# Performance work log

Measured on AMD Instinct MI355X. Metric: run time of the kernel, lower is better.

The kernel has to match this reference:

```python
import jax, jax.numpy as jnp
import numpy as np

HIDDEN = 2048
N_HEADS = 32
HEAD_DIM = HIDDEN // N_HEADS  # 64
SEQ = 2048
BATCH = 1
CHUNK = 256
TOPK = 4
THETA = 10000.0
EPS = 1e-6
NEG = jnp.float32(-1e30)


def setup_inputs() -> dict:
    key = jax.random.key(0)
    ks = jax.random.split(key, 8)
    s = 0.02
    return {
        "hidden_states": jax.random.normal(ks[0], (BATCH, SEQ, HIDDEN), jnp.float32),
        "Wq": jax.random.normal(ks[1], (HIDDEN, HIDDEN), jnp.float32) * s,
        "Wk": jax.random.normal(ks[2], (HIDDEN, HIDDEN), jnp.float32) * s,
        "Wv": jax.random.normal(ks[3], (HIDDEN, HIDDEN), jnp.float32) * s,
        "Wo": jax.random.normal(ks[4], (HIDDEN, HIDDEN), jnp.float32) * s,
        "Wg1": jax.random.normal(ks[5], (HEAD_DIM, HIDDEN), jnp.float32) * s,
        "Wg2": jax.random.normal(ks[6], (HIDDEN, HEAD_DIM), jnp.float32) * s,
        "o_norm_weight": jnp.ones((HEAD_DIM,), jnp.float32),
    }


def _rope(t):
    # t: [B, S, H, D]; non-interleaved (NeoX-style) rotary over full head dim
    D = t.shape[-1]
    pos = jnp.arange(t.shape[1], dtype=jnp.float32)
    inv_freq = 1.0 / (THETA ** (jnp.arange(0, D, 2, dtype=jnp.float32) / D))
    freqs = pos[:, None] * inv_freq[None, :]            # [S, D/2]
    cos = jnp.cos(freqs)[None, :, None, :]
    sin = jnp.sin(freqs)[None, :, None, :]
    t1, t2 = t[..., : D // 2], t[..., D // 2:]
    return jnp.concatenate([t1 * cos - t2 * sin, t1 * sin + t2 * cos], axis=-1)


def reference(hidden_states, Wq, Wk, Wv, Wo, Wg1, Wg2, o_norm_weight):
    B, S, _ = hidden_states.shape
    H, D, C = N_HEADS, HEAD_DIM, CHUNK
    NC = S // C

    q = (hidden_states @ Wq.T).reshape(B, S, H, D)
    k = (hidden_states @ Wk.T).reshape(B, S, H, D)
    v = (hidden_states @ Wv.T).reshape(B, S, H, D)
    q, k = _rope(q), _rope(k)

    # --- MoBA gating: per-chunk mean-pooled keys scored against each query ---
    kmean = k.reshape(B, NC, C, H, D).mean(axis=2)           # [B, NC, H, D]
    gate = jnp.einsum('bshd,bnhd->bhsn', q, kmean)           # [B, H, S, NC]

    pos = jnp.arange(S)
    q_chunk = pos // C                                       # [S]
    chunk_ids = jnp.arange(NC)
    future = chunk_ids[None, :] > q_chunk[:, None]           # [S, NC]
    self_blk = chunk_ids[None, :] == q_chunk[:, None]
    gate = jnp.where(future[None, None], NEG, gate)
    gate = jnp.where(self_blk[None, None], -NEG, gate)       # self block always selected

    _, topk_idx = jax.lax.top_k(gate, TOPK)                  # [B, H, S, TOPK]
    sel = jax.nn.one_hot(topk_idx, NC, dtype=jnp.bool_).any(axis=-2)  # [B, H, S, NC]

    # --- block-sparse causal attention over selected chunks ---
    allowed = jnp.take(sel, q_chunk, axis=-1)                # [B, H, S, S] key j -> chunk j//C
    causal = pos[None, :] <= pos[:, None]                    # [S, S]
    allowed = allowed & causal[None, None]

    scale = 1.0 / np.sqrt(D)
    scores = jnp.einsum('bshd,bthd->bhst', q, k) * scale
    scores = jnp.where(allowed, scores, NEG)
    p = jax.nn.softmax(scores, axis=-1)
    o = jnp.einsum('bhst,bthd->bshd', p, v)                  # [B, S, H, D]

    # --- gated RMSNorm (FusedRMSNormGated, sigmoid activation) ---
    g = ((hidden_states @ Wg1.T) @ Wg2.T).reshape(B, S, H, D)
    rms = jax.lax.rsqrt(jnp.mean(o * o, axis=-1, keepdims=True) + EPS)
    o = o * rms * o_norm_weight * jax.nn.sigmoid(g)

    return (o.reshape(B, S, H * D)) @ Wo.T
```

## Files before the change

kernel.cpp:

```cpp
#include <hip/hip_runtime.h>
#include <hip/hip_bf16.h>


typedef __attribute__((ext_vector_type(8))) short s8v;
typedef __attribute__((ext_vector_type(4))) float f4v;

#define MFMA16(A,B,C) __builtin_amdgcn_mfma_f32_16x16x32_bf16(A,B,C,0,0,0)

__device__ __forceinline__ unsigned short f2b_rne(float f){
  unsigned u = __builtin_bit_cast(unsigned, f);
  u = (u + 0x7FFFu + ((u>>16)&1u)) >> 16;
  return (unsigned short)u;
}
__device__ __forceinline__ float b2f(unsigned short h){
  unsigned u = ((unsigned)h)<<16;
  return __builtin_bit_cast(float, u);
}
__device__ __forceinline__ unsigned pack2(float a, float b){
  return (unsigned)f2b_rne(a) | ((unsigned)f2b_rne(b)<<16);
}
__device__ __forceinline__ void gld16(const void* g, void* l){
  __builtin_amdgcn_global_load_lds((const __attribute__((address_space(1))) void*)g,
                                   (__attribute__((address_space(3))) void*)l, 16, 0, 0);
}

__global__ __launch_bounds__(256) void rtab_k(double2* __restrict__ tab){
  const int i = blockIdx.x*256 + threadIdx.x;
  if (i >= 2048*32) return;
  const int d2 = i & 31, s = i >> 5;
  const double invf = 1.0 / pow(10000.0, (double)d2 / 32.0);
  const double ph = (double)s * invf;
  tab[i] = make_double2(cos(ph), sin(ph));
}

__global__ __launch_bounds__(256) void f2b4_k(const float* __restrict__ s,
                                              unsigned short* __restrict__ d, int n4){
  int i = blockIdx.x*256 + threadIdx.x;
  if (i >= n4) return;
  const float4 v = *(const float4*)(s + (size_t)i*4);
  uint2 p; p.x = pack2(v.x, v.y); p.y = pack2(v.z, v.w);
  *(uint2*)(d + (size_t)i*4) = p;
}

__global__ __launch_bounds__(256) void f2bs_k(const float* __restrict__ s,
    unsigned short* __restrict__ hi, unsigned short* __restrict__ lo, int n4){
  int i = blockIdx.x*256 + threadIdx.x;
  if (i >= n4) return;
  const float4 v = *(const float4*)(s + (size_t)i*4);
  unsigned short h0 = f2b_rne(v.x), h1 = f2b_rne(v.y), h2 = f2b_rne(v.z), h3 = f2b_rne(v.w);
  uint2 ph; ph.x = (unsigned)h0 | ((unsigned)h1<<16); ph.y = (unsigned)h2 | ((unsigned)h3<<16);
  uint2 pl; pl.x = pack2(v.x - b2f(h0), v.y - b2f(h1));
  pl.y = pack2(v.z - b2f(h2), v.w - b2f(h3));
  *(uint2*)(hi + (size_t)i*4) = ph;
  *(uint2*)(lo + (size_t)i*4) = pl;
}

__global__ __launch_bounds__(128) void wsum_k(const float* __restrict__ hs,
    const double2* __restrict__ tab, double* __restrict__ AcT, double* __restrict__ AsT){
  const int n = blockIdx.x, cq = blockIdx.y;
  const int c = cq*128 + threadIdx.x;
  double ac[32] = {}, as_[32] = {};
  for (int i = 0; i < 256; ++i) {
    const int s = n*256 + i;
    const double v = (double)hs[(size_t)s*2048 + c];
    #pragma unroll
    for (int d2 = 0; d2 < 32; ++d2) {
      const double2 t = tab[s*32 + d2];
      ac[d2]  += t.x*v;
      as_[d2] += t.y*v;
    }
  }
  #pragma unroll
  for (int d2 = 0; d2 < 32; ++d2) {
    AcT[(size_t)c*256 + n*32 + d2] = ac[d2]*(1.0/256.0);
    AsT[(size_t)c*256 + n*32 + d2] = as_[d2]*(1.0/256.0);
  }
}

__global__ __launch_bounds__(256) void transf_k(const float* __restrict__ in,
    float* __restrict__ out, int R, int C){
  __shared__ float t[64][65];
  const int c0 = blockIdx.x*64, r0 = blockIdx.y*64;
  const int tx = threadIdx.x & 63, ty4 = threadIdx.x >> 6;
  #pragma unroll
  for (int rr = 0; rr < 16; ++rr) {
    const int r = ty4*16 + rr;
    t[r][tx] = in[(size_t)(r0+r)*C + c0+tx];
  }
  __syncthreads();
  #pragma unroll
  for (int rr = 0; rr < 16; ++rr) {
    const int c = ty4*16 + rr;
    out[(size_t)(c0+c)*R + r0+tx] = t[tx][c];
  }
}

__global__ __launch_bounds__(1024) void kmean2_k(const double* __restrict__ AcT,
    const double* __restrict__ AsT, const float* __restrict__ WkT,
    double* __restrict__ Km){
  const int n = blockIdx.x, h = blockIdx.y;
  const int tid = threadIdx.x, d = tid & 63, p = tid >> 6;
  const int d2 = d & 31;
  const bool hiHalf = d >= 32;
  double a = 0.0, b = 0.0;
  #pragma unroll 4
  for (int c = p*128; c < p*128 + 128; ++c) {
    const double x  = AcT[(size_t)c*256 + n*32 + d2];
    const double y  = AsT[(size_t)c*256 + n*32 + d2];
    const double w1 = (double)WkT[(size_t)c*2048 + h*64 + d2];
    const double w2 = (double)WkT[(size_t)c*2048 + h*64 + d2 + 32];
    if (!hiHalf) { a += x*w1; b += y*w2; }
    else         { a += y*w1; b += x*w2; }
  }
  __shared__ double red[1024];
  red[tid] = hiHalf ? (a + b) : (a - b);
  __syncthreads();
  if (p < 8) red[tid] += red[tid + 512];
  __syncthreads();
  if (p < 4) red[tid] += red[tid + 256];
  __syncthreads();
  if (p < 2) red[tid] += red[tid + 128];
  __syncthreads();
  if (p == 0)
    Km[(size_t)(n*32 + h)*64 + d] = red[d] + red[d + 64];
}

__global__ __launch_bounds__(256) void gate_topk_k(const float* __restrict__ Qf,
    const double* __restrict__ Km, unsigned char* __restrict__ Allow,
    unsigned char* __restrict__ Flags){
  const int h = blockIdx.x, c = blockIdx.y, t = threadIdx.x;
  __shared__ double km[512];
  km[t]     = Km[((t>>6)*32 + h)*64 + (t&63)];
  km[t+256] = Km[(((t+256)>>6)*32 + h)*64 + (t&63)];
  __syncthreads();
  const int s = c*256 + t;
  const float* qp = Qf + (size_t)s*2048 + h*64;
  double g[8] = {};
  for (int d = 0; d < 64; ++d) {
    const double qv = (double)qp[d];
    #pragma unroll
    for (int n2 = 0; n2 < 8; ++n2) g[n2] += qv*km[n2*64+d];
  }
  double margin = 1e300;
  if (c >= 4) {
    unsigned pm = 0;
    double v[4];
    for (int rep = 0; rep < 4; ++rep) {
      double best = -1e308; int bi = 0;
      #pragma unroll
      for (int n2 = 0; n2 < 8; ++n2) {
        const bool take = (n2 < c) && !((pm>>n2)&1u) && (g[n2] > best);
        best = take ? g[n2] : best;
        bi   = take ? n2 : bi;
      }
      v[rep] = best; pm |= 1u<<bi;
    }
    margin = v[2] - v[3];
  }
  Flags[h*2048 + s] = (margin < 1e-3) ? 1 : 0;
  #pragma unroll
  for (int n2 = 0; n2 < 8; ++n2) if (n2 > c) g[n2] = -1e300;
  g[c] = 1e300;
  unsigned mask = 0;
  for (int rep = 0; rep < 4; ++rep) {
    double best = -1e308; int bi = 0;
    #pragma unroll
    for (int n2 = 0; n2 < 8; ++n2) {
      const bool take = !((mask>>n2)&1u) && (g[n2] > best);
      best = take ? g[n2] : best;
      bi   = take ? n2 : bi;
    }
    mask |= 1u<<bi;
  }
  Allow[h*2048 + s] = (unsigned char)mask;
}

__global__ __launch_bounds__(64) void repair_k(
    const float* __restrict__ hs, const float* __restrict__ Wq,
    const double2* __restrict__ tab, const double* __restrict__ Km,
    const unsigned char* __restrict__ Flags, unsigned char* __restrict__ Allow)
{
  const int s = blockIdx.x, d = threadIdx.x;
  __shared__ double qr[64];
  __shared__ double g8[8];
  for (int h = 0; h < 32; ++h) {
    if (!Flags[h*2048 + s]) continue;
    const float* hrow = hs + (size_t)s*2048;
    const float* wrow = Wq + (size_t)(h*64 + d)*2048;
    double a0=0,a1=0,a2=0,a3=0;
    for (int k = 0; k < 2048; k += 4) {
      a0 += (double)hrow[k]  *(double)wrow[k];
      a1 += (double)hrow[k+1]*(double)wrow[k+1];
      a2 += (double)hrow[k+2]*(double)wrow[k+2];
      a3 += (double)hrow[k+3]*(double)wrow[k+3];
    }
    qr[d] = (a0+a1)+(a2+a3);
    __syncthreads();
    const double2 t = tab[s*32 + (d&31)];
    const double rot = (d < 32) ? (qr[d]*t.x - qr[d+32]*t.y)
                                : (qr[d-32]*t.y + qr[d]*t.x);
    __syncthreads();
    qr[d] = rot;
    __syncthreads();
    if (d < 8) {
      double g = 0;
      const double* kmp = Km + (size_t)(d*32 + h)*64;
      for (int dd = 0; dd < 64; ++dd) g += qr[dd]*kmp[dd];
      g8[d] = g;
    }
    __syncthreads();
    if (d == 0) {
      const int c = s >> 8;
      double g[8];
      #pragma unroll
      for (int n2 = 0; n2 < 8; ++n2)
        g[n2] = (n2 > c) ? -1e300 : ((n2 == c) ? 1e300 : g8[n2]);
      unsigned mask = 0;
      for (int rep = 0; rep < 4; ++rep) {
        double best = -1e308; int bi = 0;
        #pragma unroll
        for (int n2 = 0; n2 < 8; ++n2) {
          const bool take = !((mask>>n2)&1u) && (g[n2] > best);
          best = take ? g[n2] : best;
          bi   = take ? n2 : bi;
        }
        mask |= 1u<<bi;
      }
      Allow[h*2048 + s] = (unsigned char)mask;
    }
    __syncthreads();
  }
}

__global__ __launch_bounds__(256) void gemm4_bt(
    const unsigned short* __restrict__ Ah, const unsigned short* __restrict__ Al,
    const unsigned short* __restrict__ Bh, const unsigned short* __restrict__ Bl,
    float* __restrict__ C, int M, int N, int K)
{
  alignas(16) __shared__ char SAh[16384];
  alignas(16) __shared__ char SAl[16384];
  alignas(16) __shared__ char SBh[16384];
  alignas(16) __shared__ char SBl[16384];
  const int t = threadIdx.x;
  const int wave = t>>6, lane = t&63, lg = lane>>4, lr = lane&15;
  const int wm = wave >> 1, wn = wave & 1;
  const int m0 = blockIdx.x*128, n0 = blockIdx.y*128;
  const unsigned short* Ahb = Ah + (size_t)m0*K;
  const unsigned short* Alb = Al + (size_t)m0*K;
  const unsigned short* Bhb = Bh + (size_t)n0*K;
  const unsigned short* Blb = Bl + (size_t)n0*K;
  f4v acc[4][4] = {};
  #pragma unroll 1
  for (int kt = 0; kt < K; kt += 64) {
    __syncthreads();
    #pragma unroll
    for (int i = 0; i < 4; ++i) {
      const size_t go = (size_t)(i*32 + (t>>3))*K + kt + (t&7)*8;
      gld16(Ahb + go, SAh + i*4096 + wave*1024);
      gld16(Alb + go, SAl + i*4096 + wave*1024);
      gld16(Bhb + go, SBh + i*4096 + wave*1024);
      gld16(Blb + go, SBl + i*4096 + wave*1024);
    }
    __syncthreads();
    #pragma unroll
    for (int kk = 0; kk < 2; ++kk) {
      s8v ah[4], al[4], bh[4], bl[4];
      #pragma unroll
      for (int i = 0; i < 4; ++i) {
        const int ro = (wm*64 + i*16 + lr)*128 + kk*64 + lg*16;
        ah[i] = *(const s8v*)&SAh[ro];
        al[i] = *(const s8v*)&SAl[ro];
      }
      #pragma unroll
      for (int j = 0; j < 4; ++j) {
        const int ro = (wn*64 + j*16 + lr)*128 + kk*64 + lg*16;
        bh[j] = *(const s8v*)&SBh[ro];
        bl[j] = *(const s8v*)&SBl[ro];
      }
      #pragma unroll
      for (int i = 0; i < 4; ++i)
        #pragma unroll
        for (int j = 0; j < 4; ++j) {
          f4v a = acc[i][j];
          a = MFMA16(ah[i], bh[j], a);
          a = MFMA16(ah[i], bl[j], a);
          a = MFMA16(al[i], bh[j], a);
          a = MFMA16(al[i], bl[j], a);
          acc[i][j] = a;
        }
    }
  }
  #pragma unroll
  for (int i = 0; i < 4; ++i)
    #pragma unroll
    for (int j = 0; j < 4; ++j) {
      const int row = m0 + wm*64 + i*16 + lg*4;
      const int col = n0 + wn*64 + j*16 + lr;
      #pragma unroll
      for (int r = 0; r < 4; ++r)
        C[(size_t)(row+r)*N + col] = acc[i][j][r];
    }
}

template<int BM, int BN, int WN, bool OUTBF>
__global__ __launch_bounds__(256) void gemm_bt(
    const unsigned short* __restrict__ A, const unsigned short* __restrict__ B,
    void* __restrict__ C, int M, int N, int K)
{
  alignas(16) __shared__ char AsB[BM*128];
  alignas(16) __shared__ char BsB[BN*128];
  const int t = threadIdx.x;
  const int wave = t>>6, lane = t&63, lg = lane>>4, lr = lane&15;
  const int wm = wave / WN, wn = wave % WN;
  const int m0 = blockIdx.x*BM, n0 = blockIdx.y*BN;
  const unsigned short* Ab = A + (size_t)m0*K;
  const unsigned short* Bb = B + (size_t)n0*K;
  f4v acc[4][4] = {};
  #pragma unroll 1
  for (int kt = 0; kt < K; kt += 64) {
    __syncthreads();
    #pragma unroll
    for (int i = 0; i < BM/32; ++i)
      gld16(Ab + (size_t)(i*32 + (t>>3))*K + kt + (t&7)*8, AsB + i*4096 + wave*1024);
    #pragma unroll
    for (int i = 0; i < BN/32; ++i)
      gld16(Bb + (size_t)(i*32 + (t>>3))*K + kt + (t&7)*8, BsB + i*4096 + wave*1024);
    __syncthreads();
    #pragma unroll
    for (int kk = 0; kk < 2; ++kk) {
      s8v af[4], bfr[4];
      #pragma unroll
      for (int i = 0; i < 4; ++i)
        af[i] = *(const s8v*)&AsB[(wm*64 + i*16 + lr)*128 + kk*64 + lg*16];
      #pragma unroll
      for (int j = 0; j < 4; ++j)
        bfr[j] = *(const s8v*)&BsB[(wn*64 + j*16 + lr)*128 + kk*64 + lg*16];
      #pragma unroll
      for (int i = 0; i < 4; ++i)
        #pragma unroll
        for (int j = 0; j < 4; ++j)
          acc[i][j] = MFMA16(af[i], bfr[j], acc[i][j]);
    }
  }
  #pragma unroll
  for (int i = 0; i < 4; ++i)
    #pragma unroll
    for (int j = 0; j < 4; ++j) {
      const int row = m0 + wm*64 + i*16 + lg*4;
      const int col = n0 + wn*64 + j*16 + lr;
      #pragma unroll
      for (int r = 0; r < 4; ++r) {
        if (OUTBF) ((unsigned short*)C)[(size_t)(row+r)*N + col] = f2b_rne(acc[i][j][r]);
        else       ((float*)C)[(size_t)(row+r)*N + col] = acc[i][j][r];
      }
    }
}

__global__ __launch_bounds__(256) void rope32q_k(float* __restrict__ Qf,
    unsigned short* __restrict__ Qb, const double2* __restrict__ tab){
  const int idx = blockIdx.x*256 + threadIdx.x;
  const int d2 = idx & 31, hh = (idx>>5)&31, s = idx>>10;
  const double2 t = tab[s*32 + d2];
  const float cs = (float)t.x, sn = (float)t.y;
  const size_t base = (size_t)s*2048 + hh*64 + d2;
  const float q1 = Qf[base], q2 = Qf[base+32];
  const float o1 = q1*cs - q2*sn, o2 = q1*sn + q2*cs;
  Qf[base] = o1; Qf[base+32] = o2;
  Qb[base] = f2b_rne(o1); Qb[base+32] = f2b_rne(o2);
}

__global__ __launch_bounds__(256) void rope32_k(const float* __restrict__ Kf,
    unsigned short* __restrict__ Kb, const double2* __restrict__ tab){
  const int idx = blockIdx.x*256 + threadIdx.x;
  const int d2 = idx & 31, hh = (idx>>5)&31, s = idx>>10;
  const double2 t = tab[s*32 + d2];
  const float cs = (float)t.x, sn = (float)t.y;
  const size_t base = (size_t)s*2048 + hh*64 + d2;
  const float k1 = Kf[base], k2 = Kf[base+32];
  Kb[base]    = f2b_rne(k1*cs - k2*sn);
  Kb[base+32] = f2b_rne(k1*sn + k2*cs);
}

__global__ __launch_bounds__(256) void vtrans_k(const float* __restrict__ V,
                                                unsigned short* __restrict__ Vt){
  __shared__ unsigned short tile[64][68];
  const int s0 = blockIdx.x*64, c0 = blockIdx.y*64;
  const int tx = threadIdx.x & 63, ty = threadIdx.x >> 6;
  #pragma unroll
  for (int rr = 0; rr < 16; ++rr) {
    const int r = ty*16 + rr;
    tile[tx][r] = f2b_rne(V[(size_t)(s0+r)*2048 + c0+tx]);
  }
  __syncthreads();
  #pragma unroll
  for (int rr = 0; rr < 16; ++rr) {
    const int cc = ty*16 + rr;
    Vt[(size_t)(c0+cc)*2048 + s0+tx] = tile[cc][tx];
  }
}

__global__ __launch_bounds__(256) void attn_k(
    const unsigned short* __restrict__ Qb, const unsigned short* __restrict__ Kb,
    const unsigned short* __restrict__ Vt, const float* __restrict__ Gf,
    const unsigned char* __restrict__ Allow, const float* __restrict__ Wn,
    unsigned short* __restrict__ Ob)
{
  const int h = blockIdx.x, c = blockIdx.y;
  const int t = threadIdx.x, wave = t>>6, lane = t&63, lg = lane>>4, lr = lane&15;
  const int qbase = c*256 + (blockIdx.z*4 + wave)*16;
  const size_t qrow = (size_t)(qbase + lr);
  const s8v qf0 = *(const s8v*)&Qb[qrow*2048 + h*64 + lg*8];
  const s8v qf1 = *(const s8v*)&Qb[qrow*2048 + h*64 + 32 + lg*8];
  const unsigned am = Allow[h*2048 + qrow];
  const int q = qbase + lr;
  const int laneA = ((lg&1)<<5) + lr;
  const bool hiSel = lg >= 2;

  float mx = -1e30f, ls = 0.f;
  f4v ot[4] = {};

  for (int n = 0; n <= c; ++n) {
    if (!__ballot((am>>n)&1u)) continue;
    const int okc = (am>>n)&1;
    #pragma unroll 1
    for (int t4 = 0; t4 < 4; ++t4) {
      const int kb0 = n*256 + t4*64;
      s8v kf[4][2];
      #pragma unroll
      for (int i = 0; i < 4; ++i) {
        const size_t krow = (size_t)(kb0 + i*16 + lr);
        kf[i][0] = *(const s8v*)&Kb[krow*2048 + h*64 + lg*8];
        kf[i][1] = *(const s8v*)&Kb[krow*2048 + h*64 + 32 + lg*8];
      }
      f4v st[4];
      #pragma unroll
      for (int i = 0; i < 4; ++i) {
        f4v zz = {};
        zz = MFMA16(kf[i][0], qf0, zz);
        st[i] = MFMA16(kf[i][1], qf1, zz);
      }
      float cm = -__builtin_inff();
      #pragma unroll
      for (int i = 0; i < 4; ++i)
        #pragma unroll
        for (int r = 0; r < 4; ++r) {
          float v = st[i][r]*0.125f;
          const int key = kb0 + i*16 + lg*4 + r;
          const bool ok = okc && (n != c || key <= q);
          v = ok ? v : -__builtin_inff();
          st[i][r] = v;
          cm = fmaxf(cm, v);
        }
      cm = fmaxf(cm, __shfl_xor(cm, 16));
      cm = fmaxf(cm, __shfl_xor(cm, 32));
      const float nm = fmaxf(mx, cm);
      const float al = __expf(mx - nm);
      mx = nm;
      uint2 w[4];
      float ps = 0.f;
      #pragma unroll
      for (int i = 0; i < 4; ++i) {
        const float p0 = __expf(st[i][0]-mx);
        const float p1 = __expf(st[i][1]-mx);
        const float p2 = __expf(st[i][2]-mx);
        const float p3 = __expf(st[i][3]-mx);
        ps += (p0+p1)+(p2+p3);
        w[i].x = pack2(p0,p1);
        w[i].y = pack2(p2,p3);
      }
      ps += __shfl_xor(ps, 16);
      ps += __shfl_xor(ps, 32);
      ls = ls*al + ps;
      #pragma unroll
      for (int jd = 0; jd < 4; ++jd) ot[jd] *= al;
      #pragma unroll
      for (int kk = 0; kk < 2; ++kk) {
        const unsigned a0x = __shfl(w[2*kk].x,   laneA);
        const unsigned a0y = __shfl(w[2*kk].y,   laneA);
        const unsigned b0x = __shfl(w[2*kk].x,   laneA+16);
        const unsigned b0y = __shfl(w[2*kk].y,   laneA+16);
        const unsigned a1x = __shfl(w[2*kk+1].x, laneA);
        const unsigned a1y = __shfl(w[2*kk+1].y, laneA);
        const unsigned b1x = __shfl(w[2*kk+1].x, laneA+16);
        const unsigned b1y = __shfl(w[2*kk+1].y, laneA+16);
        uint4 uu;
        uu.x = hiSel ? a1x : a0x;
        uu.y = hiSel ? a1y : a0y;
        uu.z = hiSel ? b1x : b0x;
        uu.w = hiSel ? b1y : b0y;
        const s8v pfr = __builtin_bit_cast(s8v, uu);
        s8v vfr[4];
        #pragma unroll
        for (int jd = 0; jd < 4; ++jd)
          vfr[jd] = *(const s8v*)&Vt[(size_t)(h*64 + jd*16 + lr)*2048 + kb0 + kk*32 + lg*8];
        #pragma unroll
        for (int jd = 0; jd < 4; ++jd)
          ot[jd] = MFMA16(vfr[jd], pfr, ot[jd]);
      }
    }
  }
  const float inv_ = 1.0f/ls;
  float ssum = 0.f;
  #pragma unroll
  for (int jd = 0; jd < 4; ++jd)
    #pragma unroll
    for (int r = 0; r < 4; ++r) {
      const float o = ot[jd][r]*inv_;
      ot[jd][r] = o;
      ssum += o*o;
    }
  ssum += __shfl_xor(ssum, 16);
  ssum += __shfl_xor(ssum, 32);
  const float rmsv = rsqrtf(ssum*(1.0f/64.0f) + 1e-6f);
  #pragma unroll
  for (int jd = 0; jd < 4; ++jd) {
    const float4 w4 = *(const float4*)&Wn[jd*16 + lg*4];
    const float4 g4 = *(const float4*)&Gf[qrow*2048 + h*64 + jd*16 + lg*4];
    const float o0 = ot[jd][0]*rmsv*w4.x*(1.0f/(1.0f+__expf(-g4.x)));
    const float o1 = ot[jd][1]*rmsv*w4.y*(1.0f/(1.0f+__expf(-g4.y)));
    const float o2 = ot[jd][2]*rmsv*w4.z*(1.0f/(1.0f+__expf(-g4.z)));
    const float o3 = ot[jd][3]*rmsv*w4.w*(1.0f/(1.0f+__expf(-g4.w)));
    uint2 pk; pk.x = pack2(o0,o1); pk.y = pack2(o2,o3);
    *(uint2*)&Ob[qrow*2048 + h*64 + jd*16 + lg*4] = pk;
  }
}

extern "C" void kernel_launch(void* const* d_in, const int* in_sizes, int n_in,
                              void* d_out, int out_size, void* d_ws, size_t ws_size,
                              hipStream_t stream)
{
  const float* hs  = (const float*)d_in[0];
  const float* Wq  = (const float*)d_in[1];
  const float* Wk  = (const float*)d_in[2];
  const float* Wv  = (const float*)d_in[3];
  const float* Wo  = (const float*)d_in[4];
  const float* Wg1 = (const float*)d_in[5];
  const float* Wg2 = (const float*)d_in[6];
  const float* Wn  = (const float*)d_in[7];

  const size_t S2 = (size_t)2048*2048;
  const size_t MB = (size_t)1<<20;
  char* ws = (char*)d_ws;
  double2*        tab   = (double2*)       (ws);
  unsigned short* hsh   = (unsigned short*)(ws + 1*MB);
  unsigned short* hsl   = (unsigned short*)(ws + 9*MB);
  unsigned short* Wqh   = (unsigned short*)(ws + 17*MB);
  unsigned short* Wql   = (unsigned short*)(ws + 25*MB);
  unsigned short* Wkb   = (unsigned short*)(ws + 33*MB);
  unsigned short* Wvb   = (unsigned short*)(ws + 41*MB);
  unsigned short* Wg1b  = (unsigned short*)(ws + 49*MB);
  unsigned short* Wg2b  = (unsigned short*)(ws + 49*MB + 262144);
  unsigned short* g1b   = (unsigned short*)(ws + 49*MB + 524288);
  double*         km    = (double*)        (ws + 49*MB + 786432);
  unsigned char*  allow = (unsigned char*) (ws + 49*MB + 917504);
  unsigned char*  flags = (unsigned char*) (ws + 49*MB + 983040);
  float*          qf    = (float*)         (ws + 50*MB);
  float*          kf    = (float*)         (ws + 66*MB);
  float*          vf    = (float*)         (ws + 82*MB);
  unsigned short* kb    = (unsigned short*)(ws + 17*MB);
  unsigned short* qb    = (unsigned short*)(ws + 25*MB);
  double*         AcT   = (double*)        (ws + 33*MB);
  double*         AsT   = (double*)        (ws + 37*MB);
  float*          WkT   = (float*)         (ws + 66*MB);
  unsigned short* vt    = (unsigned short*)(ws + 66*MB);
  unsigned short* ob    = (unsigned short*)(ws + 74*MB);
  float*          gf    = (float*)         (ws + 82*MB);
  unsigned short* Wob   = (unsigned short*)(ws + 50*MB);
  (void)ws_size; (void)in_sizes; (void)n_in; (void)out_size;

  rtab_k<<<256,256,0,stream>>>(tab);
  f2bs_k<<<4096,256,0,stream>>>(hs, hsh, hsl, (int)(S2/4));
  f2bs_k<<<4096,256,0,stream>>>(Wq, Wqh, Wql, (int)(S2/4));
  f2b4_k<<<4096,256,0,stream>>>(Wk, Wkb, (int)(S2/4));
  f2b4_k<<<4096,256,0,stream>>>(Wv, Wvb, (int)(S2/4));
  f2b4_k<<<128,256,0,stream>>>(Wg1, Wg1b, 64*2048/4);
  f2b4_k<<<128,256,0,stream>>>(Wg2, Wg2b, 2048*64/4);

  gemm4_bt<<<dim3(16,16),256,0,stream>>>(hsh, hsl, Wqh, Wql, qf, 2048, 2048, 2048);
  gemm_bt<128,128,2,false><<<dim3(16,16),256,0,stream>>>(hsh, Wkb, kf, 2048, 2048, 2048);
  gemm_bt<128,128,2,false><<<dim3(16,16),256,0,stream>>>(hsh, Wvb, vf, 2048, 2048, 2048);

  rope32q_k<<<8192,256,0,stream>>>(qf, qb, tab);
  rope32_k<<<8192,256,0,stream>>>(kf, kb, tab);

  wsum_k<<<dim3(8,16),128,0,stream>>>(hs, tab, AcT, AsT);
  transf_k<<<dim3(32,32),256,0,stream>>>(Wk, WkT, 2048, 2048);
  kmean2_k<<<dim3(8,32),1024,0,stream>>>(AcT, AsT, WkT, km);
  gate_topk_k<<<dim3(32,8),256,0,stream>>>(qf, km, allow, flags);
  repair_k<<<2048,64,0,stream>>>(hs, Wq, tab, km, flags, allow);

  vtrans_k<<<dim3(32,32),256,0,stream>>>(vf, vt);
  gemm_bt<256,64,1,true><<<dim3(8,1),256,0,stream>>>(hsh, Wg1b, g1b, 2048, 64, 2048);
  gemm_bt<128,128,2,false><<<dim3(16,16),256,0,stream>>>(g1b, Wg2b, gf, 2048, 2048, 64);

  attn_k<<<dim3(32,8,4),256,0,stream>>>(qb, kb, vt, gf, allow, Wn, ob);

  f2b4_k<<<4096,256,0,stream>>>(Wo, Wob, (int)(S2/4));
  gemm_bt<128,128,2,false><<<dim3(16,16),256,0,stream>>>(ob, Wob, d_out, 2048, 2048, 2048);
}
```

Measured before the change: 828.3 us.

## Compute pooled-key means with split-bf16 MFMA GEMM and store gate as bf16

Replaces the fp64 scalar kmean path (transpose of Wk plus a per-head fp64 dot-product reduction) with an fp64 weighted-sum kernel, a split hi/lo bf16 conversion, and two gemm4_bt MFMA GEMMs against a hi/lo split of Wk, followed by a small combine kernel. The wsum kernel is also reorganized to write a row-major layout suitable for the GEMM. The gate projection output is now written as bf16 instead of fp32 to halve its traffic into attention. Costs: an extra split conversion of Wk, and reduced precision in the gating scores, which could flip top-k selections (the repair kernel may compensate).

```diff
diff --git a/kernel.cpp b/kernel.cpp
--- a/kernel.cpp
+++ b/kernel.cpp
@@ -55,74 +55,56 @@
   *(uint2*)(lo + (size_t)i*4) = pl;
 }
 
-__global__ __launch_bounds__(128) void wsum_k(const float* __restrict__ hs,
-    const double2* __restrict__ tab, double* __restrict__ AcT, double* __restrict__ AsT){
-  const int n = blockIdx.x, cq = blockIdx.y;
-  const int c = cq*128 + threadIdx.x;
-  double ac[32] = {}, as_[32] = {};
+__global__ __launch_bounds__(256) void d2bs_k(const double* __restrict__ s,
+    unsigned short* __restrict__ hi, unsigned short* __restrict__ lo, int n2){
+  const int i = blockIdx.x*256 + threadIdx.x;
+  if (i >= n2) return;
+  #pragma unroll
+  for (int j = 0; j < 2; ++j) {
+    const float f = (float)s[(size_t)i*2+j];
+    const unsigned short h = f2b_rne(f);
+    hi[(size_t)i*2+j] = h;
+    lo[(size_t)i*2+j] = f2b_rne(f - b2f(h));
+  }
+}
+
+__global__ __launch_bounds__(1024) void wsum_k(const float* __restrict__ hs,
+    const double2* __restrict__ tab, double* __restrict__ Ac, double* __restrict__ As){
+  const int n = blockIdx.x, d2q = blockIdx.y;
+  const int tid = threadIdx.x;
+  const int d2base = d2q*8;
+  double ac[8][2] = {}, as_[8][2] = {};
   for (int i = 0; i < 256; ++i) {
     const int s = n*256 + i;
-    const double v = (double)hs[(size_t)s*2048 + c];
-    #pragma unroll
-    for (int d2 = 0; d2 < 32; ++d2) {
-      const double2 t = tab[s*32 + d2];
-      ac[d2]  += t.x*v;
-      as_[d2] += t.y*v;
-    }
-  }
-  #pragma unroll
-  for (int d2 = 0; d2 < 32; ++d2) {
-    AcT[(size_t)c*256 + n*32 + d2] = ac[d2]*(1.0/256.0);
-    AsT[(size_t)c*256 + n*32 + d2] = as_[d2]*(1.0/256.0);
-  }
-}
-
-__global__ __launch_bounds__(256) void transf_k(const float* __restrict__ in,
-    float* __restrict__ out, int R, int C){
-  __shared__ float t[64][65];
-  const int c0 = blockIdx.x*64, r0 = blockIdx.y*64;
-  const int tx = threadIdx.x & 63, ty4 = threadIdx.x >> 6;
-  #pragma unroll
-  for (int rr = 0; rr < 16; ++rr) {
-    const int r = ty4*16 + rr;
-    t[r][tx] = in[(size_t)(r0+r)*C + c0+tx];
-  }
-  __syncthreads();
-  #pragma unroll
-  for (int rr = 0; rr < 16; ++rr) {
-    const int c = ty4*16 + rr;
-    out[(size_t)(c0+c)*R + r0+tx] = t[tx][c];
-  }
-}
-
-__global__ __launch_bounds__(1024) void kmean2_k(const double* __restrict__ AcT,
-    const double* __restrict__ AsT, const float* __restrict__ WkT,
-    double* __restrict__ Km){
-  const int n = blockIdx.x, h = blockIdx.y;
-  const int tid = threadIdx.x, d = tid & 63, p = tid >> 6;
+    const double v0 = (double)hs[(size_t)s*2048 + tid];
+    const double v1 = (double)hs[(size_t)s*2048 + tid + 1024];
+    #pragma unroll
+    for (int j = 0; j < 8; ++j) {
+      const double2 t = tab[s*32 + d2base + j];
+      ac[j][0]  += t.x*v0; ac[j][1]  += t.x*v1;
+      as_[j][0] += t.y*v0; as_[j][1] += t.y*v1;
+    }
+  }
+  #pragma unroll
+  for (int j = 0; j < 8; ++j) {
+    const size_t row = (size_t)(n*32 + d2base + j)*2048;
+    Ac[row + tid]        = ac[j][0]*(1.0/256.0);
+    Ac[row + tid + 1024] = ac[j][1]*(1.0/256.0);
+    As[row + tid]        = as_[j][0]*(1.0/256.0);
+    As[row + tid + 1024] = as_[j][1]*(1.0/256.0);
+  }
+}
+
+__global__ __launch_bounds__(256) void kmcomb_k(const float* __restrict__ Cc,
+    const float* __restrict__ Cs, double* __restrict__ Km){
+  const int i = blockIdx.x*256 + threadIdx.x;
+  const int d = i & 63, h = (i>>6) & 31, n = i >> 11;
   const int d2 = d & 31;
-  const bool hiHalf = d >= 32;
-  double a = 0.0, b = 0.0;
-  #pragma unroll 4
-  for (int c = p*128; c < p*128 + 128; ++c) {
-    const double x  = AcT[(size_t)c*256 + n*32 + d2];
-    const double y  = AsT[(size_t)c*256 + n*32 + d2];
-    const double w1 = (double)WkT[(size_t)c*2048 + h*64 + d2];
-    const double w2 = (double)WkT[(size_t)c*2048 + h*64 + d2 + 32];
-    if (!hiHalf) { a += x*w1; b += y*w2; }
-    else         { a += y*w1; b += x*w2; }
-  }
-  __shared__ double red[1024];
-  red[tid] = hiHalf ? (a + b) : (a - b);
-  __syncthreads();
-  if (p < 8) red[tid] += red[tid + 512];
-  __syncthreads();
-  if (p < 4) red[tid] += red[tid + 256];
-  __syncthreads();
-  if (p < 2) red[tid] += red[tid + 128];
-  __syncthreads();
-  if (p == 0)
-    Km[(size_t)(n*32 + h)*64 + d] = red[d] + red[d + 64];
+  const size_t row = (size_t)(n*32 + d2)*2048;
+  double v;
+  if (d < 32) v = (double)Cc[row + h*64 + d2] - (double)Cs[row + h*64 + d2 + 32];
+  else        v = (double)Cs[row + h*64 + d2] + (double)Cc[row + h*64 + d2 + 32];
+  Km[(size_t)(n*32 + h)*64 + d] = v;
 }
 
 __global__ __launch_bounds__(256) void gate_topk_k(const float* __restrict__ Qf,
@@ -401,7 +383,7 @@
 
 __global__ __launch_bounds__(256) void attn_k(
     const unsigned short* __restrict__ Qb, const unsigned short* __restrict__ Kb,
-    const unsigned short* __restrict__ Vt, const float* __restrict__ Gf,
+    const unsigned short* __restrict__ Vt, const unsigned short* __restrict__ Gb,
     const unsigned char* __restrict__ Allow, const float* __restrict__ Wn,
     unsigned short* __restrict__ Ob)
 {
@@ -515,11 +497,11 @@
   #pragma unroll
   for (int jd = 0; jd < 4; ++jd) {
     const float4 w4 = *(const float4*)&Wn[jd*16 + lg*4];
-    const float4 g4 = *(const float4*)&Gf[qrow*2048 + h*64 + jd*16 + lg*4];
-    const float o0 = ot[jd][0]*rmsv*w4.x*(1.0f/(1.0f+__expf(-g4.x)));
-    const float o1 = ot[jd][1]*rmsv*w4.y*(1.0f/(1.0f+__expf(-g4.y)));
-    const float o2 = ot[jd][2]*rmsv*w4.z*(1.0f/(1.0f+__expf(-g4.z)));
-    const float o3 = ot[jd][3]*rmsv*w4.w*(1.0f/(1.0f+__expf(-g4.w)));
+    const ushort4 gu = *(const ushort4*)&Gb[qrow*2048 + h*64 + jd*16 + lg*4];
+    const float o0 = ot[jd][0]*rmsv*w4.x*(1.0f/(1.0f+__expf(-b2f(gu.x))));
+    const float o1 = ot[jd][1]*rmsv*w4.y*(1.0f/(1.0f+__expf(-b2f(gu.y))));
+    const float o2 = ot[jd][2]*rmsv*w4.z*(1.0f/(1.0f+__expf(-b2f(gu.z))));
+    const float o3 = ot[jd][3]*rmsv*w4.w*(1.0f/(1.0f+__expf(-b2f(gu.w))));
     uint2 pk; pk.x = pack2(o0,o1); pk.y = pack2(o2,o3);
     *(uint2*)&Ob[qrow*2048 + h*64 + jd*16 + lg*4] = pk;
   }
@@ -542,58 +524,69 @@
   const size_t MB = (size_t)1<<20;
   char* ws = (char*)d_ws;
   double2*        tab   = (double2*)       (ws);
-  unsigned short* hsh   = (unsigned short*)(ws + 1*MB);
-  unsigned short* hsl   = (unsigned short*)(ws + 9*MB);
-  unsigned short* Wqh   = (unsigned short*)(ws + 17*MB);
-  unsigned short* Wql   = (unsigned short*)(ws + 25*MB);
-  unsigned short* Wkb   = (unsigned short*)(ws + 33*MB);
-  unsigned short* Wvb   = (unsigned short*)(ws + 41*MB);
-  unsigned short* Wg1b  = (unsigned short*)(ws + 49*MB);
-  unsigned short* Wg2b  = (unsigned short*)(ws + 49*MB + 262144);
-  unsigned short* g1b   = (unsigned short*)(ws + 49*MB + 524288);
-  double*         km    = (double*)        (ws + 49*MB + 786432);
-  unsigned char*  allow = (unsigned char*) (ws + 49*MB + 917504);
-  unsigned char*  flags = (unsigned char*) (ws + 49*MB + 983040);
-  float*          qf    = (float*)         (ws + 50*MB);
-  float*          kf    = (float*)         (ws + 66*MB);
-  float*          vf    = (float*)         (ws + 82*MB);
-  unsigned short* kb    = (unsigned short*)(ws + 17*MB);
-  unsigned short* qb    = (unsigned short*)(ws + 25*MB);
-  double*         AcT   = (double*)        (ws + 33*MB);
-  double*         AsT   = (double*)        (ws + 37*MB);
-  float*          WkT   = (float*)         (ws + 66*MB);
-  unsigned short* vt    = (unsigned short*)(ws + 66*MB);
-  unsigned short* ob    = (unsigned short*)(ws + 74*MB);
-  float*          gf    = (float*)         (ws + 82*MB);
-  unsigned short* Wob   = (unsigned short*)(ws + 50*MB);
+  unsigned short* Wg1b  = (unsigned short*)(ws + 1*MB);
+  unsigned short* Wg2b  = (unsigned short*)(ws + 1*MB + 262144);
+  unsigned short* g1b   = (unsigned short*)(ws + 1*MB + 524288);
+  double*         km    = (double*)        (ws + 1*MB + 786432);
+  unsigned char*  allow = (unsigned char*) (ws + 1*MB + 917504);
+  unsigned char*  flags = (unsigned char*) (ws + 1*MB + 983040);
+  unsigned short* hsh   = (unsigned short*)(ws + 2*MB);
+  unsigned short* hsl   = (unsigned short*)(ws + 10*MB);
+  unsigned short* Wqh   = (unsigned short*)(ws + 18*MB);
+  unsigned short* Wql   = (unsigned short*)(ws + 26*MB);
+  unsigned short* Wkh   = (unsigned short*)(ws + 34*MB);
+  unsigned short* Wkl   = (unsigned short*)(ws + 42*MB);
+  unsigned short* Wvb   = (unsigned short*)(ws + 50*MB);
+  float*          qf    = (float*)         (ws + 58*MB);
+  float*          kf    = (float*)         (ws + 74*MB);
+  float*          vf    = (float*)         (ws + 90*MB);
+  double*         Ac    = (double*)        (ws + 106*MB);
+  double*         As    = (double*)        (ws + 110*MB);
+  unsigned short* Ach   = (unsigned short*)(ws + 18*MB);
+  unsigned short* Acl   = (unsigned short*)(ws + 19*MB);
+  unsigned short* Ash   = (unsigned short*)(ws + 20*MB);
+  unsigned short* Asl   = (unsigned short*)(ws + 21*MB);
+  float*          Cc    = (float*)         (ws + 22*MB);
+  float*          Cs    = (float*)         (ws + 24*MB);
+  unsigned short* qb    = (unsigned short*)(ws + 26*MB);
+  unsigned short* kb    = (unsigned short*)(ws + 42*MB);
+  unsigned short* vt    = (unsigned short*)(ws + 74*MB);
+  unsigned short* ob    = (unsigned short*)(ws + 82*MB);
+  unsigned short* gb    = (unsigned short*)(ws + 90*MB);
+  unsigned short* Wob   = (unsigned short*)(ws + 98*MB);
   (void)ws_size; (void)in_sizes; (void)n_in; (void)out_size;
 
   rtab_k<<<256,256,0,stream>>>(tab);
   f2bs_k<<<4096,256,0,stream>>>(hs, hsh, hsl, (int)(S2/4));
   f2bs_k<<<4096,256,0,stream>>>(Wq, Wqh, Wql, (int)(S2/4));
-  f2b4_k<<<4096,256,0,stream>>>(Wk, Wkb, (int)(S2/4));
+  f2bs_k<<<4096,256,0,stream>>>(Wk, Wkh, Wkl, (int)(S2/4));
   f2b4_k<<<4096,256,0,stream>>>(Wv, Wvb, (int)(S2/4));
   f2b4_k<<<128,256,0,stream>>>(Wg1, Wg1b, 64*2048/4);
   f2b4_k<<<128,256,0,stream>>>(Wg2, Wg2b, 2048*64/4);
 
   gemm4_bt<<<dim3(16,16),256,0,stream>>>(hsh, hsl, Wqh, Wql, qf, 2048, 2048, 2048);
-  gemm_bt<128,128,2,false><<<dim3(16,16),256,0,stream>>>(hsh, Wkb, kf, 2048, 2048, 2048);
+  gemm_bt<128,128,2,false><<<dim3(16,16),256,0,stream>>>(hsh, Wkh, kf, 2048, 2048, 2048);
   gemm_bt<128,128,2,false><<<dim3(16,16),256,0,stream>>>(hsh, Wvb, vf, 2048, 2048, 2048);
 
   rope32q_k<<<8192,256,0,stream>>>(qf, qb, tab);
+
+  wsum_k<<<dim3(8,4),1024,0,stream>>>(hs, tab, Ac, As);
+  d2bs_k<<<1024,256,0,stream>>>(Ac, Ach, Acl, 262144);
+  d2bs_k<<<1024,256,0,stream>>>(As, Ash, Asl, 262144);
+  gemm4_bt<<<dim3(2,16),256,0,stream>>>(Ach, Acl, Wkh, Wkl, Cc, 256, 2048, 2048);
+  gemm4_bt<<<dim3(2,16),256,0,stream>>>(Ash, Asl, Wkh, Wkl, Cs, 256, 2048, 2048);
+  kmcomb_k<<<64,256,0,stream>>>(Cc, Cs, km);
+
   rope32_k<<<8192,256,0,stream>>>(kf, kb, tab);
 
-  wsum_k<<<dim3(8,16),128,0,stream>>>(hs, tab, AcT, AsT);
-  transf_k<<<dim3(32,32),256,0,stream>>>(Wk, WkT, 2048, 2048);
-  kmean2_k<<<dim3(8,32),1024,0,stream>>>(AcT, AsT, WkT, km);
   gate_topk_k<<<dim3(32,8),256,0,stream>>>(qf, km, allow, flags);
   repair_k<<<2048,64,0,stream>>>(hs, Wq, tab, km, flags, allow);
 
   vtrans_k<<<dim3(32,32),256,0,stream>>>(vf, vt);
   gemm_bt<256,64,1,true><<<dim3(8,1),256,0,stream>>>(hsh, Wg1b, g1b, 2048, 64, 2048);
-  gemm_bt<128,128,2,false><<<dim3(16,16),256,0,stream>>>(g1b, Wg2b, gf, 2048, 2048, 64);
-
-  attn_k<<<dim3(32,8,4),256,0,stream>>>(qb, kb, vt, gf, allow, Wn, ob);
+  gemm_bt<128,128,2,true><<<dim3(16,16),256,0,stream>>>(g1b, Wg2b, gb, 2048, 2048, 64);
+
+  attn_k<<<dim3(32,8,4),256,0,stream>>>(qb, kb, vt, gb, allow, Wn, ob);
 
   f2b4_k<<<4096,256,0,stream>>>(Wo, Wob, (int)(S2/4));
   gemm_bt<128,128,2,false><<<dim3(16,16),256,0,stream>>>(ob, Wob, d_out, 2048, 2048, 2048);
```

New measurement: 915.6 us. 10.5% more time.
